# Optimization experiments

Hardware: AMD Instinct MI355X
Metric: run time of the kernel (lower is better)

The kernel has to match this reference:

```python
import jax, jax.numpy as jnp
import numpy as np

B, T, C = 4, 4096, 256
H = 4
D = C // H
EPS = 1e-5


def layer_norm(x, w, b):
    mean = x.mean(axis=-1, keepdims=True)
    var = x.var(axis=-1, keepdims=True)
    return w * (x - mean) / jnp.sqrt(var + EPS) + b


def setup_inputs() -> dict:
    key = jax.random.key(0)
    ks = jax.random.split(key, 8)
    s = lambda n: 1.0 / np.sqrt(n)
    return {
        "x": jax.random.normal(ks[0], (B, T, C), jnp.float32),
        "qkv_w": jax.random.normal(ks[1], (C, 3 * C), jnp.float32) * s(C),
        "qkv_b": jnp.zeros((3 * C,), jnp.float32),
        "proj_w": jax.random.normal(ks[2], (C, C), jnp.float32) * s(C),
        "proj_b": jnp.zeros((C,), jnp.float32),
        "n1_w": jnp.ones((C,), jnp.float32),
        "n1_b": jnp.zeros((C,), jnp.float32),
        "ffn_w1": jax.random.normal(ks[3], (C, 3 * C), jnp.float32) * s(C),
        "ffn_b1": jnp.zeros((3 * C,), jnp.float32),
        "ffn_w2": jax.random.normal(ks[4], (3 * C, C), jnp.float32) * s(3 * C),
        "ffn_b2": jnp.zeros((C,), jnp.float32),
        "n2_w": jnp.ones((C,), jnp.float32),
        "n2_b": jnp.zeros((C,), jnp.float32),
    }


def reference(x, qkv_w, qkv_b, proj_w, proj_b, n1_w, n1_b,
              ffn_w1, ffn_b1, ffn_w2, ffn_b2, n2_w, n2_b):
    scale = D ** -0.5
    qkv = (x @ qkv_w + qkv_b).reshape(B, T, 3, H, D)
    qkv = jnp.transpose(qkv, (2, 0, 3, 1, 4))  # [3, B, H, T, D]
    q, k, v = qkv[0], qkv[1], qkv[2]
    attn = jnp.einsum('bhtd,bhsd->bhts', q, k) * scale  # [B,H,T,T]
    attn = jax.nn.softmax(attn, axis=-1)
    out = jnp.einsum('bhts,bhsd->bhtd', attn, v)
    out = jnp.transpose(out, (0, 2, 1, 3)).reshape(B, T, C)
    attn_out = out @ proj_w + proj_b
    x = layer_norm(x + attn_out, n1_w, n1_b)
    h = jax.nn.gelu(x @ ffn_w1 + ffn_b1, approximate=False)
    ffn_out = h @ ffn_w2 + ffn_b2
    x = layer_norm(x + ffn_out, n2_w, n2_b)
    return x
```

## Files before the change

kernel.cpp:

```cpp
#include <hip/hip_runtime.h>
#include <cstdint>
#include <cstddef>

typedef __bf16 bf16;
typedef __bf16 bf16x8 __attribute__((ext_vector_type(8)));
typedef __bf16 bf16x4 __attribute__((ext_vector_type(4)));
typedef _Float16 f16;
typedef _Float16 f16x4 __attribute__((ext_vector_type(4)));
typedef _Float16 f16x8 __attribute__((ext_vector_type(8)));
typedef __fp16 fp16x2 __attribute__((ext_vector_type(2)));
typedef float f32x4 __attribute__((ext_vector_type(4)));

#define DEV static __device__ __forceinline__
#if __has_builtin(__builtin_amdgcn_exp2f)
#define EXP2(x) __builtin_amdgcn_exp2f(x)
#else
#define EXP2(x) exp2f(x)
#endif
#define QSCALE 0.18033688011112042f

DEV float gelu_exact(float v) {
  return 0.5f * v * (1.0f + erff(v * 0.70710678118654752f));
}

__global__ void cvt_w_kernel(const float* __restrict__ qkv_w, bf16* __restrict__ qwt,
                             const float* __restrict__ proj_w, bf16* __restrict__ pwt,
                             const float* __restrict__ f1w, bf16* __restrict__ f1wt,
                             const float* __restrict__ f2w, bf16* __restrict__ f2wt,
                             const float* __restrict__ x, bf16* __restrict__ xb) {
  int blk = blockIdx.x;
  const int tid = threadIdx.x;
  if (blk >= 160) {
    const size_t i = ((size_t)(blk - 160) * 256 + tid) * 8;
    const float4 a0 = *(const float4*)(x + i);
    const float4 a1 = *(const float4*)(x + i + 4);
    bf16x8 v;
    v[0] = (bf16)a0.x; v[1] = (bf16)a0.y; v[2] = (bf16)a0.z; v[3] = (bf16)a0.w;
    v[4] = (bf16)a1.x; v[5] = (bf16)a1.y; v[6] = (bf16)a1.z; v[7] = (bf16)a1.w;
    *(bf16x8*)(xb + i) = v;
    return;
  }
  const float* w; bf16* o; int K, N;
  if (blk < 48)       { w = qkv_w;  o = qwt;  K = 256; N = 768; }
  else if (blk < 64)  { w = proj_w; o = pwt;  K = 256; N = 256; blk -= 48; }
  else if (blk < 112) { w = f1w;    o = f1wt; K = 256; N = 768; blk -= 64; }
  else                { w = f2w;    o = f2wt; K = 768; N = 256; blk -= 112; }
  const int ntiles = N >> 6;
  const int kt = blk / ntiles, nt = blk - kt * ntiles;
  const int k0 = kt * 64, n0 = nt * 64;
  __shared__ float tile[64][65];
#pragma unroll
  for (int j = 0; j < 4; ++j) {
    const int c = j * 256 + tid;
    const int row = c >> 4, c4 = (c & 15) * 4;
    const float4 v = *(const float4*)(w + (size_t)(k0 + row) * N + n0 + c4);
    tile[row][c4] = v.x; tile[row][c4 + 1] = v.y;
    tile[row][c4 + 2] = v.z; tile[row][c4 + 3] = v.w;
  }
  __syncthreads();
#pragma unroll
  for (int j = 0; j < 4; ++j) {
    const int c = j * 256 + tid;
    const int n = c >> 4, k4 = (c & 15) * 4;
    bf16x4 ov;
#pragma unroll
    for (int i = 0; i < 4; ++i) ov[i] = (bf16)tile[k4 + i][n];
    *(bf16x4*)(o + (size_t)(n0 + n) * K + k0 + k4) = ov;
  }
}

__global__ __launch_bounds__(256, 3)
void gemm_qkv_kernel(const bf16* __restrict__ A, const bf16* __restrict__ Wt,
                     const float* __restrict__ bias, bf16* __restrict__ qb,
                     bf16* __restrict__ kb, f16* __restrict__ vt) {
  const int tid = threadIdx.x;
  const int wave = tid >> 6, lane = tid & 63;
  const int quad = lane >> 4, l15 = lane & 15;
  const int m0 = blockIdx.y * 128, n0 = blockIdx.x * 128;
  const int mw = (wave >> 1) * 64, nw = (wave & 1) * 64;
  const int K = 256;

  __shared__ bf16 lA[128 * 72];
  __shared__ bf16 lB[128 * 72];

  f32x4 acc[4][4] = {};

  for (int k0 = 0; k0 < K; k0 += 64) {
#pragma unroll
    for (int j = 0; j < 4; ++j) {
      const int c = j * 256 + tid;
      const int row = c >> 3, kc = (c & 7) * 8;
      *(uint4*)(lA + row * 72 + kc) =
          *(const uint4*)(A + (size_t)(m0 + row) * K + k0 + kc);
      *(uint4*)(lB + row * 72 + kc) =
          *(const uint4*)(Wt + (size_t)(n0 + row) * K + k0 + kc);
    }
    __syncthreads();
#pragma unroll
    for (int ks = 0; ks < 2; ++ks) {
      bf16x8 af[4], bfm[4];
#pragma unroll
      for (int i = 0; i < 4; ++i)
        af[i] = *(const bf16x8*)(lA + (mw + i * 16 + l15) * 72 + ks * 32 + quad * 8);
#pragma unroll
      for (int j = 0; j < 4; ++j)
        bfm[j] = *(const bf16x8*)(lB + (nw + j * 16 + l15) * 72 + ks * 32 + quad * 8);
#pragma unroll
      for (int i = 0; i < 4; ++i)
#pragma unroll
        for (int j = 0; j < 4; ++j)
          acc[i][j] = __builtin_amdgcn_mfma_f32_16x16x32_bf16(af[i], bfm[j],
                                                              acc[i][j], 0, 0, 0);
    }
    __syncthreads();
  }

  const bool isV = (n0 >= 512);
#pragma unroll
  for (int i = 0; i < 4; ++i) {
#pragma unroll
    for (int j = 0; j < 4; ++j) {
      const int n = n0 + nw + j * 16 + l15;
      const float bs = bias[n];
      if (isV) {
        const int m = m0 + mw + i * 16 + quad * 4;
        const int b = m >> 12, t = m & 4095;
        const int h = (n >> 6) & 3, d = n & 63;
        const int tp = (t & ~31) | (((t >> 2) & 3) << 3) | (((t >> 4) & 1) << 2);
        f16x4 hv;
#pragma unroll
        for (int r = 0; r < 4; ++r) hv[r] = (f16)(acc[i][j][r] + bs);
        *(f16x4*)(vt + (size_t)((b * 4 + h) * 64 + d) * 4096 + tp) = hv;
      } else {
        const int s = n >> 8, cc = n & 255, h = cc >> 6, d = cc & 63;
#pragma unroll
        for (int r = 0; r < 4; ++r) {
          const int m = m0 + mw + i * 16 + quad * 4 + r;
          const int b = m >> 12, t = m & 4095;
          const float v = acc[i][j][r] + bs;
          const size_t idx = (size_t)((b * 4 + h) * 4096 + t) * 64 + d;
          if (s == 0) qb[idx] = (bf16)(v * QSCALE);
          else        kb[idx] = (bf16)v;
        }
      }
    }
  }
}

__global__ __launch_bounds__(256, 2)
void attn_kernel(const bf16* __restrict__ q, const bf16* __restrict__ k,
                 const f16* __restrict__ vt, bf16* __restrict__ o0,
                 bf16* __restrict__ o1, float* __restrict__ pD) {
  const int tid = threadIdx.x;
  const int wave = tid >> 6, lane = tid & 63;
  const int quad = lane >> 4, l15 = lane & 15;
  const int bh = blockIdx.y;
  const int q0 = blockIdx.x * 128;
  const int z = blockIdx.z;
  const int kvbase = z * 2048;
  __shared__ bf16 lK[2][64 * 72];
  __shared__ f16  lV[2][64 * 72];

  bf16x8 qa0[2], qa1[2];
#pragma unroll
  for (int s = 0; s < 2; ++s) {
    const bf16* qp =
        q + ((size_t)bh * 4096 + q0 + wave * 32 + s * 16 + l15) * 64 + quad * 8;
    qa0[s] = *(const bf16x8*)(qp);
    qa1[s] = *(const bf16x8*)(qp + 32);
  }

  const int row0 = tid >> 3, off = (tid & 7) * 8;
  const bf16* kp = k + ((size_t)bh * 4096 + kvbase + row0) * 64 + off;
  const f16*  vp = vt + ((size_t)bh * 64 + row0) * 4096 + kvbase + off;
  const int lidx = row0 * 72 + off;

  *(uint4*)(lK[0] + lidx)            = *(const uint4*)(kp);
  *(uint4*)(lK[0] + lidx + 32 * 72)  = *(const uint4*)(kp + 32 * 64);
  *(uint4*)(lV[0] + lidx)            = *(const uint4*)(vp);
  *(uint4*)(lV[0] + lidx + 32 * 72)  = *(const uint4*)(vp + 32 * 4096);

  f32x4 accO[2][4] = {};
  f32x4 accD[2] = {};
  const f16x8 vone8 = {(f16)1.0f, (f16)1.0f, (f16)1.0f, (f16)1.0f,
                       (f16)1.0f, (f16)1.0f, (f16)1.0f, (f16)1.0f};
  uint4 pk0, pk1, pv0, pv1;

  for (int it = 0; it < 32; ++it) {
    const int cur = it & 1;
    if (it + 1 < 32) {
      const bf16* kn = kp + (size_t)(it + 1) * 64 * 64;
      const f16*  vn = vp + (it + 1) * 64;
      pk0 = *(const uint4*)(kn);
      pk1 = *(const uint4*)(kn + 32 * 64);
      pv0 = *(const uint4*)(vn);
      pv1 = *(const uint4*)(vn + 32 * 4096);
    }
    __syncthreads();

    f32x4 sf[2][4];
    __builtin_amdgcn_s_setprio(1);
#pragma unroll
    for (int c = 0; c < 4; ++c) {
      const bf16x8 kb0 = *(const bf16x8*)(lK[cur] + (c * 16 + l15) * 72 + quad * 8);
      const bf16x8 kb1 = *(const bf16x8*)(lK[cur] + (c * 16 + l15) * 72 + 32 + quad * 8);
#pragma unroll
      for (int s = 0; s < 2; ++s) {
        f32x4 t = {};
        t = __builtin_amdgcn_mfma_f32_16x16x32_bf16(kb0, qa0[s], t, 0, 0, 0);
        t = __builtin_amdgcn_mfma_f32_16x16x32_bf16(kb1, qa1[s], t, 0, 0, 0);
        sf[s][c] = t;
      }
    }
    __builtin_amdgcn_s_setprio(0);

    f16x8 pa[2][2];
#pragma unroll
    for (int s = 0; s < 2; ++s)
#pragma unroll
      for (int c2 = 0; c2 < 2; ++c2) {
        union { fp16x2 h2[4]; f16x8 h8; } u;
        u.h2[0] = __builtin_amdgcn_cvt_pkrtz(EXP2(sf[s][2 * c2][0]),
                                             EXP2(sf[s][2 * c2][1]));
        u.h2[1] = __builtin_amdgcn_cvt_pkrtz(EXP2(sf[s][2 * c2][2]),
                                             EXP2(sf[s][2 * c2][3]));
        u.h2[2] = __builtin_amdgcn_cvt_pkrtz(EXP2(sf[s][2 * c2 + 1][0]),
                                             EXP2(sf[s][2 * c2 + 1][1]));
        u.h2[3] = __builtin_amdgcn_cvt_pkrtz(EXP2(sf[s][2 * c2 + 1][2]),
                                             EXP2(sf[s][2 * c2 + 1][3]));
        pa[s][c2] = u.h8;
      }

    __builtin_amdgcn_s_setprio(1);
#pragma unroll
    for (int s = 0; s < 2; ++s)
#pragma unroll
      for (int c2 = 0; c2 < 2; ++c2)
        accD[s] = __builtin_amdgcn_mfma_f32_16x16x32_f16(pa[s][c2], vone8,
                                                         accD[s], 0, 0, 0);

#pragma unroll
    for (int c2 = 0; c2 < 2; ++c2) {
#pragma unroll
      for (int n = 0; n < 4; ++n) {
        const f16x8 vb =
            *(const f16x8*)(lV[cur] + (n * 16 + l15) * 72 + c2 * 32 + quad * 8);
#pragma unroll
        for (int s = 0; s < 2; ++s)
          accO[s][n] = __builtin_amdgcn_mfma_f32_16x16x32_f16(pa[s][c2], vb,
                                                              accO[s][n], 0, 0, 0);
      }
    }
    __builtin_amdgcn_s_setprio(0);

    if (it + 1 < 32) {
      *(uint4*)(lK[cur ^ 1] + lidx)           = pk0;
      *(uint4*)(lK[cur ^ 1] + lidx + 32 * 72) = pk1;
      *(uint4*)(lV[cur ^ 1] + lidx)           = pv0;
      *(uint4*)(lV[cur ^ 1] + lidx + 32 * 72) = pv1;
    }
  }

  bf16* po = z ? o1 : o0;
  const int b = bh >> 2, h = bh & 3;
#pragma unroll
  for (int s = 0; s < 2; ++s) {
    float inv[4];
#pragma unroll
    for (int r = 0; r < 4; ++r) inv[r] = 1.0f / accD[s][r];
#pragma unroll
    for (int r = 0; r < 4; ++r) {
      const int t = q0 + wave * 32 + s * 16 + quad * 4 + r;
      if (l15 == 0) pD[(size_t)(z * 16 + bh) * 4096 + t] = accD[s][r];
#pragma unroll
      for (int n = 0; n < 4; ++n)
        po[(size_t)(b * 4096 + t) * 256 + h * 64 + n * 16 + l15] =
            (bf16)(accO[s][n][r] * inv[r]);
    }
  }
}

__global__ __launch_bounds__(256)
void attn_combine_kernel(bf16* __restrict__ o0, const bf16* __restrict__ o1,
                         const float* __restrict__ pD) {
  const size_t base = ((size_t)blockIdx.x * 256 + threadIdx.x) * 8;
  const int row = (int)(base >> 8);
  const int b = row >> 12, t = row & 4095;
  const int h = ((int)(base >> 6)) & 3;
  const float d0 = pD[(size_t)(b * 4 + h) * 4096 + t];
  const float d1 = pD[(size_t)(16 + b * 4 + h) * 4096 + t];
  const float w = 1.0f / (d0 + d1);
  const float w0 = d0 * w, w1 = d1 * w;
  const bf16x8 a = *(const bf16x8*)(o0 + base);
  const bf16x8 c = *(const bf16x8*)(o1 + base);
  bf16x8 r;
#pragma unroll
  for (int i = 0; i < 8; ++i)
    r[i] = (bf16)((float)a[i] * w0 + (float)c[i] * w1);
  *(bf16x8*)(o0 + base) = r;
}

__global__ __launch_bounds__(256, 3)
void gemm_ffn1_kernel(const bf16* __restrict__ A, const bf16* __restrict__ Wt,
                      const float* __restrict__ bias, bf16* __restrict__ ob) {
  const int tid = threadIdx.x;
  const int wave = tid >> 6, lane = tid & 63;
  const int quad = lane >> 4, l15 = lane & 15;
  const int m0 = blockIdx.y * 128, n0 = blockIdx.x * 128;
  const int mw = (wave >> 1) * 64, nw = (wave & 1) * 64;
  const int K = 256;

  __shared__ bf16 lA[128 * 72];
  __shared__ bf16 lB[128 * 72];

  f32x4 acc[4][4] = {};

  for (int k0 = 0; k0 < K; k0 += 64) {
#pragma unroll
    for (int j = 0; j < 4; ++j) {
      const int c = j * 256 + tid;
      const int row = c >> 3, kc = (c & 7) * 8;
      *(uint4*)(lA + row * 72 + kc) =
          *(const uint4*)(A + (size_t)(m0 + row) * K + k0 + kc);
      *(uint4*)(lB + row * 72 + kc) =
          *(const uint4*)(Wt + (size_t)(n0 + row) * K + k0 + kc);
    }
    __syncthreads();
#pragma unroll
    for (int ks = 0; ks < 2; ++ks) {
      bf16x8 af[4], bfm[4];
#pragma unroll
      for (int i = 0; i < 4; ++i)
        af[i] = *(const bf16x8*)(lA + (mw + i * 16 + l15) * 72 + ks * 32 + quad * 8);
#pragma unroll
      for (int j = 0; j < 4; ++j)
        bfm[j] = *(const bf16x8*)(lB + (nw + j * 16 + l15) * 72 + ks * 32 + quad * 8);
#pragma unroll
      for (int i = 0; i < 4; ++i)
#pragma unroll
        for (int j = 0; j < 4; ++j)
          acc[i][j] = __builtin_amdgcn_mfma_f32_16x16x32_bf16(af[i], bfm[j],
                                                              acc[i][j], 0, 0, 0);
    }
    __syncthreads();
  }

#pragma unroll
  for (int i = 0; i < 4; ++i) {
#pragma unroll
    for (int j = 0; j < 4; ++j) {
      const int n = n0 + nw + j * 16 + l15;
      const float bs = bias[n];
#pragma unroll
      for (int r = 0; r < 4; ++r) {
        const int m = m0 + mw + i * 16 + quad * 4 + r;
        ob[(size_t)m * 768 + n] = (bf16)gelu_exact(acc[i][j][r] + bs);
      }
    }
  }
}

template <int KTILES, bool RESID_BF16, bool WRITE_F, bool WRITE_B>
__global__ __launch_bounds__(256, 3)
void gemm_ln_kernel(const bf16* __restrict__ A, const bf16* __restrict__ Wt,
                    const float* __restrict__ bias, const void* __restrict__ Rv,
                    const float* __restrict__ lw, const float* __restrict__ lb,
                    float* __restrict__ outf, bf16* __restrict__ outb) {
  const int tid = threadIdx.x;
  const int wave = tid >> 6, lane = tid & 63;
  const int quad = lane >> 4, l15 = lane & 15;
  const int m0 = blockIdx.x * 32;
  const int nw = wave * 64;
  const int K = KTILES * 64;
  __shared__ bf16 lA[32 * 72];
  __shared__ bf16 lB[256 * 72];
  __shared__ float lnsum[4][32];
  __shared__ float lnsq[4][32];
  __shared__ float lnstat[32][2];
  f32x4 acc[2][4] = {};

  for (int kt = 0; kt < KTILES; ++kt) {
    const int k0 = kt * 64;
    {
      const int row = tid >> 3, kc = (tid & 7) * 8;
      *(uint4*)(lA + row * 72 + kc) =
          *(const uint4*)(A + (size_t)(m0 + row) * K + k0 + kc);
    }
#pragma unroll
    for (int j = 0; j < 8; ++j) {
      const int c = j * 256 + tid;
      const int row = c >> 3, kc = (c & 7) * 8;
      *(uint4*)(lB + row * 72 + kc) =
          *(const uint4*)(Wt + (size_t)row * K + k0 + kc);
    }
    __syncthreads();
#pragma unroll
    for (int ks = 0; ks < 2; ++ks) {
      bf16x8 af[2], bfm[4];
#pragma unroll
      for (int i = 0; i < 2; ++i)
        af[i] = *(const bf16x8*)(lA + (i * 16 + l15) * 72 + ks * 32 + quad * 8);
#pragma unroll
      for (int j = 0; j < 4; ++j)
        bfm[j] = *(const bf16x8*)(lB + (nw + j * 16 + l15) * 72 + ks * 32 + quad * 8);
#pragma unroll
      for (int i = 0; i < 2; ++i)
#pragma unroll
        for (int j = 0; j < 4; ++j)
          acc[i][j] = __builtin_amdgcn_mfma_f32_16x16x32_bf16(af[i], bfm[j],
                                                              acc[i][j], 0, 0, 0);
    }
    __syncthreads();
  }

  float bv[4], lwv[4], lbv[4];
#pragma unroll
  for (int j = 0; j < 4; ++j) {
    const int col = nw + 16 * j + l15;
    bv[j] = bias[col]; lwv[j] = lw[col]; lbv[j] = lb[col];
  }
#pragma unroll
  for (int i = 0; i < 2; ++i) {
    float ps[4] = {}, pq[4] = {};
#pragma unroll
    for (int j = 0; j < 4; ++j) {
#pragma unroll
      for (int r = 0; r < 4; ++r) {
        const int m = m0 + 16 * i + 4 * quad + r;
        const size_t ri = (size_t)m * 256 + nw + 16 * j + l15;
        const float rv = RESID_BF16 ? (float)((const bf16*)Rv)[ri]
                                    : ((const float*)Rv)[ri];
        const float v = acc[i][j][r] + bv[j] + rv;
        acc[i][j][r] = v;
        ps[r] += v;
        pq[r] += v * v;
      }
    }
#pragma unroll
    for (int r = 0; r < 4; ++r) {
#pragma unroll
      for (int mm = 1; mm < 16; mm <<= 1) {
        ps[r] += __shfl_xor(ps[r], mm, 64);
        pq[r] += __shfl_xor(pq[r], mm, 64);
      }
      if (l15 == 0) {
        lnsum[wave][16 * i + 4 * quad + r] = ps[r];
        lnsq[wave][16 * i + 4 * quad + r] = pq[r];
      }
    }
  }
  __syncthreads();
  if (tid < 32) {
    const float s = lnsum[0][tid] + lnsum[1][tid] + lnsum[2][tid] + lnsum[3][tid];
    const float sq = lnsq[0][tid] + lnsq[1][tid] + lnsq[2][tid] + lnsq[3][tid];
    const float mean = s * (1.0f / 256.0f);
    const float var = sq * (1.0f / 256.0f) - mean * mean;
    lnstat[tid][0] = mean;
    lnstat[tid][1] = rsqrtf(var + 1e-5f);
  }
  __syncthreads();
#pragma unroll
  for (int i = 0; i < 2; ++i) {
#pragma unroll
    for (int r = 0; r < 4; ++r) {
      const int row = 16 * i + 4 * quad + r;
      const float mean = lnstat[row][0], rstd = lnstat[row][1];
#pragma unroll
      for (int j = 0; j < 4; ++j) {
        const float ov = (acc[i][j][r] - mean) * rstd * lwv[j] + lbv[j];
        const size_t gi = (size_t)(m0 + row) * 256 + nw + 16 * j + l15;
        if constexpr (WRITE_F) outf[gi] = ov;
        if constexpr (WRITE_B) outb[gi] = (bf16)ov;
      }
    }
  }
}

extern "C" void kernel_launch(void* const* d_in, const int* in_sizes, int n_in,
                              void* d_out, int out_size, void* d_ws, size_t ws_size,
                              hipStream_t stream) {
  const float* x      = (const float*)d_in[0];
  const float* qkv_w  = (const float*)d_in[1];
  const float* qkv_b  = (const float*)d_in[2];
  const float* proj_w = (const float*)d_in[3];
  const float* proj_b = (const float*)d_in[4];
  const float* n1_w   = (const float*)d_in[5];
  const float* n1_b   = (const float*)d_in[6];
  const float* ffn_w1 = (const float*)d_in[7];
  const float* ffn_b1 = (const float*)d_in[8];
  const float* ffn_w2 = (const float*)d_in[9];
  const float* ffn_b2 = (const float*)d_in[10];
  const float* n2_w   = (const float*)d_in[11];
  const float* n2_b   = (const float*)d_in[12];
  float* out = (float*)d_out;

  char* ws = (char*)d_ws;
  bf16*  qwt  = (bf16*)(ws + 0);
  bf16*  pwt  = (bf16*)(ws + 393216);
  bf16*  f1wt = (bf16*)(ws + 524288);
  bf16*  f2wt = (bf16*)(ws + 917504);
  bf16*  qb   = (bf16*)(ws + 1310720);
  bf16*  kb   = (bf16*)(ws + 9699328);
  f16*   vtb  = (f16*)(ws + 18087936);
  bf16*  attn = (bf16*)(ws + 26476544);
  bf16*  x1b  = (bf16*)(ws + 34865152);
  bf16*  hbuf = (bf16*)(ws + 1310720);
  bf16*  xb   = (bf16*)(ws + 34865152);
  bf16*  po1  = (bf16*)(ws + 34865152);
  float* pden = (float*)(ws + 43253760);

  cvt_w_kernel<<<2208, 256, 0, stream>>>(qkv_w, qwt, proj_w, pwt,
                                         ffn_w1, f1wt, ffn_w2, f2wt, x, xb);
  gemm_qkv_kernel<<<dim3(6, 128), 256, 0, stream>>>(xb, qwt, qkv_b, qb, kb, vtb);
  attn_kernel<<<dim3(32, 16, 2), 256, 0, stream>>>(qb, kb, vtb, attn, po1, pden);
  attn_combine_kernel<<<2048, 256, 0, stream>>>(attn, po1, pden);
  gemm_ln_kernel<4, false, false, true><<<512, 256, 0, stream>>>(
      attn, pwt, proj_b, x, n1_w, n1_b, nullptr, x1b);
  gemm_ffn1_kernel<<<dim3(6, 128), 256, 0, stream>>>(x1b, f1wt, ffn_b1, hbuf);
  gemm_ln_kernel<12, true, true, false><<<512, 256, 0, stream>>>(
      hbuf, f2wt, ffn_b2, x1b, n2_w, n2_b, out, nullptr);
}
```

Baseline: 241.6 us.

## Fuse attention split-combine into proj GEMM and register-prefetch GEMM tiles

Removes the separate attention combine kernel and instead merges the two split-KV partial outputs, weighted by their denominators, while loading the A tile inside the projection+LayerNorm GEMM. All three GEMM kernel types also prefetch the next K-tile from global memory into registers while MFMAs run on the current LDS tile, and drop the trailing barrier. This saves a launch and a full read/write pass over the attention output, and hides global load latency. The cost is more registers per thread, especially the 8 uint4 prefetch buffers in gemm_ln, which may hurt occupancy at launch bounds of 3. The po1 buffer is moved to a separate workspace offset so it no longer aliases x1b.

New measurement: 340.2 us. 40.8% more time.

```diff
diff --git a/kernel.cpp b/kernel.cpp
--- a/kernel.cpp
+++ b/kernel.cpp
@@ -84,18 +84,35 @@
   __shared__ bf16 lB[128 * 72];
 
   f32x4 acc[4][4] = {};
+  uint4 pa4[4], pb4[4];
+
+#pragma unroll
+  for (int j = 0; j < 4; ++j) {
+    const int c = j * 256 + tid;
+    const int row = c >> 3, kc = (c & 7) * 8;
+    pa4[j] = *(const uint4*)(A + (size_t)(m0 + row) * K + kc);
+    pb4[j] = *(const uint4*)(Wt + (size_t)(n0 + row) * K + kc);
+  }
 
   for (int k0 = 0; k0 < K; k0 += 64) {
+    __syncthreads();
 #pragma unroll
     for (int j = 0; j < 4; ++j) {
       const int c = j * 256 + tid;
       const int row = c >> 3, kc = (c & 7) * 8;
-      *(uint4*)(lA + row * 72 + kc) =
-          *(const uint4*)(A + (size_t)(m0 + row) * K + k0 + kc);
-      *(uint4*)(lB + row * 72 + kc) =
-          *(const uint4*)(Wt + (size_t)(n0 + row) * K + k0 + kc);
-    }
-    __syncthreads();
+      *(uint4*)(lA + row * 72 + kc) = pa4[j];
+      *(uint4*)(lB + row * 72 + kc) = pb4[j];
+    }
+    __syncthreads();
+    if (k0 + 64 < K) {
+#pragma unroll
+      for (int j = 0; j < 4; ++j) {
+        const int c = j * 256 + tid;
+        const int row = c >> 3, kc = (c & 7) * 8;
+        pa4[j] = *(const uint4*)(A + (size_t)(m0 + row) * K + k0 + 64 + kc);
+        pb4[j] = *(const uint4*)(Wt + (size_t)(n0 + row) * K + k0 + 64 + kc);
+      }
+    }
 #pragma unroll
     for (int ks = 0; ks < 2; ++ks) {
       bf16x8 af[4], bfm[4];
@@ -112,7 +129,6 @@
           acc[i][j] = __builtin_amdgcn_mfma_f32_16x16x32_bf16(af[i], bfm[j],
                                                               acc[i][j], 0, 0, 0);
     }
-    __syncthreads();
   }
 
   const bool isV = (n0 >= 512);
@@ -280,26 +296,6 @@
   }
 }
 
-__global__ __launch_bounds__(256)
-void attn_combine_kernel(bf16* __restrict__ o0, const bf16* __restrict__ o1,
-                         const float* __restrict__ pD) {
-  const size_t base = ((size_t)blockIdx.x * 256 + threadIdx.x) * 8;
-  const int row = (int)(base >> 8);
-  const int b = row >> 12, t = row & 4095;
-  const int h = ((int)(base >> 6)) & 3;
-  const float d0 = pD[(size_t)(b * 4 + h) * 4096 + t];
-  const float d1 = pD[(size_t)(16 + b * 4 + h) * 4096 + t];
-  const float w = 1.0f / (d0 + d1);
-  const float w0 = d0 * w, w1 = d1 * w;
-  const bf16x8 a = *(const bf16x8*)(o0 + base);
-  const bf16x8 c = *(const bf16x8*)(o1 + base);
-  bf16x8 r;
-#pragma unroll
-  for (int i = 0; i < 8; ++i)
-    r[i] = (bf16)((float)a[i] * w0 + (float)c[i] * w1);
-  *(bf16x8*)(o0 + base) = r;
-}
-
 __global__ __launch_bounds__(256, 3)
 void gemm_ffn1_kernel(const bf16* __restrict__ A, const bf16* __restrict__ Wt,
                       const float* __restrict__ bias, bf16* __restrict__ ob) {
@@ -314,18 +310,35 @@
   __shared__ bf16 lB[128 * 72];
 
   f32x4 acc[4][4] = {};
+  uint4 pa4[4], pb4[4];
+
+#pragma unroll
+  for (int j = 0; j < 4; ++j) {
+    const int c = j * 256 + tid;
+    const int row = c >> 3, kc = (c & 7) * 8;
+    pa4[j] = *(const uint4*)(A + (size_t)(m0 + row) * K + kc);
+    pb4[j] = *(const uint4*)(Wt + (size_t)(n0 + row) * K + kc);
+  }
 
   for (int k0 = 0; k0 < K; k0 += 64) {
+    __syncthreads();
 #pragma unroll
     for (int j = 0; j < 4; ++j) {
       const int c = j * 256 + tid;
       const int row = c >> 3, kc = (c & 7) * 8;
-      *(uint4*)(lA + row * 72 + kc) =
-          *(const uint4*)(A + (size_t)(m0 + row) * K + k0 + kc);
-      *(uint4*)(lB + row * 72 + kc) =
-          *(const uint4*)(Wt + (size_t)(n0 + row) * K + k0 + kc);
-    }
-    __syncthreads();
+      *(uint4*)(lA + row * 72 + kc) = pa4[j];
+      *(uint4*)(lB + row * 72 + kc) = pb4[j];
+    }
+    __syncthreads();
+    if (k0 + 64 < K) {
+#pragma unroll
+      for (int j = 0; j < 4; ++j) {
+        const int c = j * 256 + tid;
+        const int row = c >> 3, kc = (c & 7) * 8;
+        pa4[j] = *(const uint4*)(A + (size_t)(m0 + row) * K + k0 + 64 + kc);
+        pb4[j] = *(const uint4*)(Wt + (size_t)(n0 + row) * K + k0 + 64 + kc);
+      }
+    }
 #pragma unroll
     for (int ks = 0; ks < 2; ++ks) {
       bf16x8 af[4], bfm[4];
@@ -342,7 +355,6 @@
           acc[i][j] = __builtin_amdgcn_mfma_f32_16x16x32_bf16(af[i], bfm[j],
                                                               acc[i][j], 0, 0, 0);
     }
-    __syncthreads();
   }
 
 #pragma unroll
@@ -360,9 +372,10 @@
   }
 }
 
-template <int KTILES, bool RESID_BF16, bool WRITE_F, bool WRITE_B>
+template <int KTILES, bool COMBINE, bool RESID_BF16, bool WRITE_F, bool WRITE_B>
 __global__ __launch_bounds__(256, 3)
-void gemm_ln_kernel(const bf16* __restrict__ A, const bf16* __restrict__ Wt,
+void gemm_ln_kernel(const bf16* __restrict__ A, const bf16* __restrict__ A2,
+                    const float* __restrict__ pD, const bf16* __restrict__ Wt,
                     const float* __restrict__ bias, const void* __restrict__ Rv,
                     const float* __restrict__ lw, const float* __restrict__ lb,
                     float* __restrict__ outf, bf16* __restrict__ outb) {
@@ -379,21 +392,71 @@
   __shared__ float lnstat[32][2];
   f32x4 acc[2][4] = {};
 
-  for (int kt = 0; kt < KTILES; ++kt) {
-    const int k0 = kt * 64;
-    {
-      const int row = tid >> 3, kc = (tid & 7) * 8;
-      *(uint4*)(lA + row * 72 + kc) =
-          *(const uint4*)(A + (size_t)(m0 + row) * K + k0 + kc);
+  const int arow = tid >> 3, akc = (tid & 7) * 8;
+  const int am = m0 + arow;
+  const int ab = am >> 12, at = am & 4095;
+
+  uint4 pb[8];
+  bf16x8 pa0, pa1;
+  float pd0 = 0.f, pd1 = 0.f;
+
+  {
+    if constexpr (COMBINE) {
+      const int h = akc >> 6;
+      pa0 = *(const bf16x8*)(A  + (size_t)am * K + akc);
+      pa1 = *(const bf16x8*)(A2 + (size_t)am * K + akc);
+      pd0 = pD[(size_t)(ab * 4 + h) * 4096 + at];
+      pd1 = pD[(size_t)(16 + ab * 4 + h) * 4096 + at];
+    } else {
+      pa0 = *(const bf16x8*)(A + (size_t)am * K + akc);
     }
 #pragma unroll
     for (int j = 0; j < 8; ++j) {
       const int c = j * 256 + tid;
       const int row = c >> 3, kc = (c & 7) * 8;
-      *(uint4*)(lB + row * 72 + kc) =
-          *(const uint4*)(Wt + (size_t)row * K + k0 + kc);
-    }
-    __syncthreads();
+      pb[j] = *(const uint4*)(Wt + (size_t)row * K + kc);
+    }
+  }
+
+  for (int kt = 0; kt < KTILES; ++kt) {
+    const int k0 = kt * 64;
+    __syncthreads();
+    if constexpr (COMBINE) {
+      const float ws = 1.0f / (pd0 + pd1);
+      const float w0 = pd0 * ws, w1 = pd1 * ws;
+      bf16x8 cv;
+#pragma unroll
+      for (int i = 0; i < 8; ++i)
+        cv[i] = (bf16)((float)pa0[i] * w0 + (float)pa1[i] * w1);
+      *(bf16x8*)(lA + arow * 72 + akc) = cv;
+    } else {
+      *(bf16x8*)(lA + arow * 72 + akc) = pa0;
+    }
+#pragma unroll
+    for (int j = 0; j < 8; ++j) {
+      const int c = j * 256 + tid;
+      const int row = c >> 3, kc = (c & 7) * 8;
+      *(uint4*)(lB + row * 72 + kc) = pb[j];
+    }
+    __syncthreads();
+    if (kt + 1 < KTILES) {
+      const int kn = k0 + 64;
+      if constexpr (COMBINE) {
+        const int h = (kn + akc) >> 6;
+        pa0 = *(const bf16x8*)(A  + (size_t)am * K + kn + akc);
+        pa1 = *(const bf16x8*)(A2 + (size_t)am * K + kn + akc);
+        pd0 = pD[(size_t)(ab * 4 + h) * 4096 + at];
+        pd1 = pD[(size_t)(16 + ab * 4 + h) * 4096 + at];
+      } else {
+        pa0 = *(const bf16x8*)(A + (size_t)am * K + kn + akc);
+      }
+#pragma unroll
+      for (int j = 0; j < 8; ++j) {
+        const int c = j * 256 + tid;
+        const int row = c >> 3, kc = (c & 7) * 8;
+        pb[j] = *(const uint4*)(Wt + (size_t)row * K + kn + kc);
+      }
+    }
 #pragma unroll
     for (int ks = 0; ks < 2; ++ks) {
       bf16x8 af[2], bfm[4];
@@ -410,7 +473,6 @@
           acc[i][j] = __builtin_amdgcn_mfma_f32_16x16x32_bf16(af[i], bfm[j],
                                                               acc[i][j], 0, 0, 0);
     }
-    __syncthreads();
   }
 
   float bv[4], lwv[4], lbv[4];
@@ -506,17 +568,16 @@
   bf16*  x1b  = (bf16*)(ws + 34865152);
   bf16*  hbuf = (bf16*)(ws + 1310720);
   bf16*  xb   = (bf16*)(ws + 34865152);
-  bf16*  po1  = (bf16*)(ws + 34865152);
-  float* pden = (float*)(ws + 43253760);
+  bf16*  po1  = (bf16*)(ws + 43253760);
+  float* pden = (float*)(ws + 51642368);
 
   cvt_w_kernel<<<2208, 256, 0, stream>>>(qkv_w, qwt, proj_w, pwt,
                                          ffn_w1, f1wt, ffn_w2, f2wt, x, xb);
   gemm_qkv_kernel<<<dim3(6, 128), 256, 0, stream>>>(xb, qwt, qkv_b, qb, kb, vtb);
   attn_kernel<<<dim3(32, 16, 2), 256, 0, stream>>>(qb, kb, vtb, attn, po1, pden);
-  attn_combine_kernel<<<2048, 256, 0, stream>>>(attn, po1, pden);
-  gemm_ln_kernel<4, false, false, true><<<512, 256, 0, stream>>>(
-      attn, pwt, proj_b, x, n1_w, n1_b, nullptr, x1b);
+  gemm_ln_kernel<4, true, false, false, true><<<512, 256, 0, stream>>>(
+      attn, po1, pden, pwt, proj_b, x, n1_w, n1_b, nullptr, x1b);
   gemm_ffn1_kernel<<<dim3(6, 128), 256, 0, stream>>>(x1b, f1wt, ffn_b1, hbuf);
-  gemm_ln_kernel<12, true, true, false><<<512, 256, 0, stream>>>(
-      hbuf, f2wt, ffn_b2, x1b, n2_w, n2_b, out, nullptr);
-}
+  gemm_ln_kernel<12, false, true, true, false><<<512, 256, 0, stream>>>(
+      hbuf, nullptr, nullptr, f2wt, ffn_b2, x1b, n2_w, n2_b, out, nullptr);
+}
```
